# Performance work log

Hardware: AMD Instinct MI355X
Metric: run time of the kernel (lower is better)

## Reference

```python
import jax, jax.numpy as jnp
import numpy as np

# dims
H = 1024          # hidden_size
E = 2048          # d_inner = 2*H
NH = 32           # nheads = E/64
P = 64            # headdim
N = 128           # d_state
G = 1             # ngroups
K = 4             # d_conv
Q = 128           # SSD chunk length
FF = 4096         # intermediate_size
EPS = 1e-6        # rms_norm_eps
NEPS = 1e-5       # mamba gated-norm eps
CONV_DIM = E + 2 * G * N            # 2304
D_IN = 2 * E + 2 * G * N + NH       # 4384


def rmsnorm(x, w, eps):
    v = jnp.mean(x.astype(jnp.float32) ** 2, axis=-1, keepdims=True)
    return (x.astype(jnp.float32) * jax.lax.rsqrt(v + eps)).astype(x.dtype) * w


def segsum(x):
    # x: [..., T] -> [..., T, T] with out[i,j] = sum_{j<k<=i} x[k], -inf above diag
    T = x.shape[-1]
    cs = jnp.cumsum(x, axis=-1)
    s = cs[..., :, None] - cs[..., None, :]
    mask = jnp.tril(jnp.ones((T, T), dtype=bool))
    return jnp.where(mask, s, -jnp.inf)


def ssd(x, dt, A_log, B, C):
    # x:[b,l,nh,p], dt:[b,l,nh], B,C:[b,l,N] (ngroups=1, shared over heads)
    b, l, nh, p = x.shape
    A = -jnp.exp(A_log)                      # [nh]
    dA = dt * A                              # [b,l,nh]
    xd = x * dt[..., None]                   # discretized input
    c = l // Q
    xd = xd.reshape(b, c, Q, nh, p)
    dAc = dA.reshape(b, c, Q, nh).transpose(0, 3, 1, 2)   # [b,h,c,q]
    Bc = B.reshape(b, c, Q, N)
    Cc = C.reshape(b, c, Q, N)
    A_cs = jnp.cumsum(dAc, axis=-1)                        # [b,h,c,q]
    Lm = jnp.exp(segsum(dAc))                              # [b,h,c,q,q]
    # intra-chunk (diagonal blocks)
    Y_diag = jnp.einsum('bcqn,bcsn,bhcqs,bcshp->bcqhp', Cc, Bc, Lm, xd)
    # per-chunk final states
    decay_states = jnp.exp(A_cs[..., -1:] - A_cs)          # [b,h,c,q]
    states = jnp.einsum('bcqn,bhcq,bcqhp->bchpn', Bc, decay_states, xd)
    # inter-chunk recurrence (initial state = 0)
    A_last = jnp.pad(A_cs[..., -1], ((0, 0), (0, 0), (1, 0)))   # [b,h,c+1]
    decay_chunk = jnp.exp(segsum(A_last))                       # [b,h,c+1,c+1]
    states = jnp.concatenate([jnp.zeros_like(states[:, :1]), states], axis=1)
    new_states = jnp.einsum('bhzc,bchpn->bzhpn', decay_chunk, states)[:, :-1]
    Y_off = jnp.einsum('bcqn,bchpn,bhcq->bcqhp', Cc, new_states, jnp.exp(A_cs))
    return (Y_diag + Y_off).reshape(b, l, nh, p)


def mamba2(h, w_in, w_conv, b_conv, dt_bias, A_log, D, w_mnorm, w_out):
    b, l, _ = h.shape
    zxbcdt = h @ w_in.T                         # [b,l,D_IN]
    z, xBC, dt = jnp.split(zxbcdt, [E, E + CONV_DIM], axis=-1)
    # causal depthwise conv (kernel K) over channels of xBC
    pad = jnp.pad(xBC, ((0, 0), (K - 1, 0), (0, 0)))
    xBC = sum(pad[:, k:k + l, :] * w_conv[:, k] for k in range(K)) + b_conv
    xBC = jax.nn.silu(xBC)
    x, B, C = jnp.split(xBC, [E, E + G * N], axis=-1)
    dt = jax.nn.softplus(dt + dt_bias)          # [b,l,NH]
    xh = x.reshape(b, l, NH, P)
    y = ssd(xh, dt, A_log, B, C)
    y = y + D[None, None, :, None] * xh         # per-head skip
    y = y.reshape(b, l, E)
    y = rmsnorm(y * jax.nn.silu(z), w_mnorm, NEPS)   # gated RMSNorm
    return y @ w_out.T


def setup_inputs() -> dict:
    key = jax.random.key(0)
    ks = jax.random.split(key, 12)
    dt0 = jax.random.uniform(ks[0], (NH,), minval=0.001, maxval=0.1)
    dt_bias = dt0 + jnp.log(-jnp.expm1(-dt0))   # inverse softplus
    return {
        'hidden_states': jax.random.normal(ks[1], (2, 2048, H), dtype=jnp.float32),
        'w_ln1': jnp.ones((H,), jnp.float32),
        'w_in': 0.02 * jax.random.normal(ks[2], (D_IN, H), dtype=jnp.float32),
        'w_conv': 0.1 * jax.random.normal(ks[3], (CONV_DIM, K), dtype=jnp.float32),
        'b_conv': jnp.zeros((CONV_DIM,), jnp.float32),
        'dt_bias': dt_bias,
        'A_log': jnp.log(jax.random.uniform(ks[4], (NH,), minval=1.0, maxval=16.0)),
        'D': jnp.ones((NH,), jnp.float32),
        'w_mnorm': jnp.ones((E,), jnp.float32),
        'w_out': 0.02 * jax.random.normal(ks[5], (H, E), dtype=jnp.float32),
        'w_ln2': jnp.ones((H,), jnp.float32),
        'w_gate': 0.02 * jax.random.normal(ks[6], (FF, H), dtype=jnp.float32),
        'w_up': 0.02 * jax.random.normal(ks[7], (FF, H), dtype=jnp.float32),
        'w_down': 0.02 * jax.random.normal(ks[8], (H, FF), dtype=jnp.float32),
    }


def reference(hidden_states, w_ln1, w_in, w_conv, b_conv, dt_bias, A_log, D,
              w_mnorm, w_out, w_ln2, w_gate, w_up, w_down):
    residual = hidden_states
    h = rmsnorm(hidden_states, w_ln1, EPS)
    h = mamba2(h, w_in, w_conv, b_conv, dt_bias, A_log, D, w_mnorm, w_out)
    hidden = residual + h
    residual = hidden
    h = rmsnorm(hidden, w_ln2, EPS)
    h = (jax.nn.silu(h @ w_gate.T) * (h @ w_up.T)) @ w_down.T
    return residual + h
```

## Files before the change

### kernel.cpp

```cpp
#include <hip/hip_runtime.h>

#define DEV static __device__ __forceinline__

typedef short bf16x8 __attribute__((ext_vector_type(8)));
typedef float floatx4 __attribute__((ext_vector_type(4)));
typedef unsigned short ushort4v __attribute__((ext_vector_type(4)));
typedef unsigned short ushort8v __attribute__((ext_vector_type(8)));

DEV unsigned short f32_bf16(float f) {
  unsigned int u = __builtin_bit_cast(unsigned int, f);
  u = u + 0x7fffu + ((u >> 16) & 1u);
  return (unsigned short)(u >> 16);
}
DEV float bf2f(unsigned short u) {
  unsigned int v = ((unsigned int)u) << 16;
  return __builtin_bit_cast(float, v);
}
DEV float sigmoidf_(float x) { return 1.0f / (1.0f + __expf(-x)); }
DEV float siluf_(float x) { return x * sigmoidf_(x); }

#define GLD_LDS16(g, l)                                                              \
  __builtin_amdgcn_global_load_lds((const __attribute__((address_space(1))) void*)(g), \
                                   (__attribute__((address_space(3))) void*)(l), 16, 0, 0)

template <int MODE, int BN>
__global__ __launch_bounds__(256) void gemm128(
    const unsigned short* __restrict__ A, const unsigned short* __restrict__ B,
    void* __restrict__ Cv, const unsigned short* __restrict__ other,
    int K, int lda, int ldb, int ldc, long long bsA, long long bsB, long long bsC) {
  constexpr int NBG = BN / 64;
  constexpr int NJ = BN / 32;
  constexpr int BUFSZ = 4096 + BN * 32;
  __shared__ unsigned short S[2 * BUFSZ];
  A += (long long)blockIdx.z * bsA;
  B += (long long)blockIdx.z * bsB;
  const long long coff = (long long)blockIdx.z * bsC;
  const int tid = threadIdx.x;
  const int w = tid >> 6, lane = tid & 63;

  const int nbx = gridDim.x, nby = gridDim.y;
  const int GM = 4;
  int bid = blockIdx.y * nbx + blockIdx.x;
  int gid = bid / (GM * nbx);
  int rem = bid - gid * (GM * nbx);
  int gsz = min(GM, nby - gid * GM);
  int mtile = gid * GM + rem % gsz;
  int ntile = rem / gsz;
  const int m0 = mtile << 7, n0 = ntile * BN;

  const int srow = lane >> 2;
  const int schunk = ((lane & 3) ^ (srow & 3)) * 8;
  const unsigned short* ag0 = A + (long long)(m0 + w * 32 + srow) * lda + schunk;
  const unsigned short* ag1 = ag0 + (long long)16 * lda;
  const unsigned short* bgp[NBG];
#pragma unroll
  for (int ii = 0; ii < NBG; ++ii)
    bgp[ii] = B + (long long)(n0 + w * (BN / 4) + srow + 16 * ii) * ldb + schunk;

  auto STAGE = [&](int buf, int k0) {
    unsigned short* as_ = S + buf * BUFSZ;
    unsigned short* bs_ = as_ + 4096;
    GLD_LDS16(ag0 + k0, as_ + w * 1024 + lane * 8);
    GLD_LDS16(ag1 + k0, as_ + w * 1024 + lane * 8 + 512);
#pragma unroll
    for (int ii = 0; ii < NBG; ++ii)
      GLD_LDS16(bgp[ii] + k0, bs_ + w * (NBG * 512) + ii * 512 + lane * 8);
  };

  const int wr = (w >> 1) << 6;
  const int wc = (w & 1) * (BN / 2);
  const int fr = lane & 15;
  const int slot = (((lane >> 4) ^ (fr & 3))) << 3;
  const int r0 = (lane >> 4) << 2;

  floatx4 acc[4][NJ];
#pragma unroll
  for (int i = 0; i < 4; ++i)
#pragma unroll
    for (int j = 0; j < NJ; ++j) acc[i][j] = (floatx4){0.f, 0.f, 0.f, 0.f};

  const int nsteps = K >> 5;
  STAGE(0, 0);
  if (nsteps > 1) STAGE(1, 32);

  for (int t = 0; t < nsteps; ++t) {
    if (t < nsteps - 1) {
      if constexpr (NBG == 2) {
        asm volatile("s_waitcnt vmcnt(4)" ::: "memory");
      } else {
        asm volatile("s_waitcnt vmcnt(6)" ::: "memory");
      }
    } else {
      asm volatile("s_waitcnt vmcnt(0)" ::: "memory");
    }
    __builtin_amdgcn_s_barrier();
    __builtin_amdgcn_sched_barrier(0);
    const unsigned short* Ab = S + (t & 1) * BUFSZ;
    const unsigned short* Bb = Ab + 4096;
    bf16x8 af[4], bf_[NJ];
#pragma unroll
    for (int i = 0; i < 4; ++i)
      af[i] = *(const bf16x8*)(Ab + (wr + i * 16 + fr) * 32 + slot);
#pragma unroll
    for (int j = 0; j < NJ; ++j)
      bf_[j] = *(const bf16x8*)(Bb + (wc + j * 16 + fr) * 32 + slot);
#pragma unroll
    for (int i = 0; i < 4; ++i)
#pragma unroll
      for (int j = 0; j < NJ; ++j)
        acc[i][j] = __builtin_amdgcn_mfma_f32_16x16x32_bf16(af[i], bf_[j], acc[i][j], 0, 0, 0);
    __builtin_amdgcn_sched_barrier(0);
    __builtin_amdgcn_s_barrier();
    if (t + 2 < nsteps) STAGE(t & 1, (t + 2) * 32);
  }

  if constexpr (MODE == 0) {
#pragma unroll
    for (int i = 0; i < 4; ++i) {
#pragma unroll
      for (int j = 0; j < NJ; ++j) {
        long long base = (long long)(m0 + wr + i * 16 + r0) * ldc + (n0 + wc + j * 16 + fr);
#pragma unroll
        for (int r = 0; r < 4; ++r) {
          ((float*)Cv)[coff + base + (long long)r * ldc] = acc[i][j][r];
        }
      }
    }
  } else {
    constexpr int PAD = BN + 4;
    float* scr = (float*)S;
    const int row_l = tid >> 3;
    const int col0 = (tid & 7) * 8;
    __syncthreads();
#pragma unroll
    for (int pass = 0; pass < 4; ++pass) {
      if ((w >> 1) == (pass >> 1)) {
#pragma unroll
        for (int ii = 0; ii < 2; ++ii) {
          int i = (pass & 1) * 2 + ii;
          int rl = i * 16 + r0 - (pass & 1) * 32;
#pragma unroll
          for (int j = 0; j < NJ; ++j) {
            int col = wc + j * 16 + fr;
#pragma unroll
            for (int r = 0; r < 4; ++r) scr[(rl + r) * PAD + col] = acc[i][j][r];
          }
        }
      }
      __syncthreads();
      long long grow = m0 + pass * 32 + row_l;
      long long gbase = coff + grow * ldc + n0;
      const float* srow_p = scr + row_l * PAD;
#pragma unroll
      for (int k = 0; k < BN / 64; ++k) {
        int col = col0 + k * 64;
        float v[8];
        *(float4*)&v[0] = *(const float4*)(srow_p + col);
        *(float4*)&v[4] = *(const float4*)(srow_p + col + 4);
        ushort8v o;
        if constexpr (MODE == 2) {
          ushort8v uo = *(const ushort8v*)(other + gbase + col);
#pragma unroll
          for (int e = 0; e < 8; ++e) o[e] = f32_bf16(siluf_(v[e]) * bf2f(uo[e]));
        } else {
#pragma unroll
          for (int e = 0; e < 8; ++e) o[e] = f32_bf16(v[e]);
        }
        *(ushort8v*)((unsigned short*)Cv + gbase + col) = o;
      }
      __syncthreads();
    }
  }
}

__global__ __launch_bounds__(256, 2) void gemm128_dual(
    const unsigned short* __restrict__ A, const unsigned short* __restrict__ Bg,
    const unsigned short* __restrict__ Bu, unsigned short* __restrict__ C,
    int K, int lda, int ldb, int ldc) {
  __shared__ unsigned short S[2 * 12288];
  const int tid = threadIdx.x;
  const int w = tid >> 6, lane = tid & 63;
  const int nbx = gridDim.x, nby = gridDim.y;
  const int GM = 4;
  int bid = blockIdx.y * nbx + blockIdx.x;
  int gid = bid / (GM * nbx);
  int rem = bid - gid * (GM * nbx);
  int gsz = min(GM, nby - gid * GM);
  int mtile = gid * GM + rem % gsz;
  int ntile = rem / gsz;
  const int m0 = mtile << 7, n0 = ntile << 7;

  const int srow = lane >> 2;
  const int schunk = ((lane & 3) ^ (srow & 3)) * 8;
  const unsigned short* ag0 = A + (long long)(m0 + w * 32 + srow) * lda + schunk;
  const unsigned short* ag1 = ag0 + (long long)16 * lda;
  const unsigned short* gg0 = Bg + (long long)(n0 + w * 32 + srow) * ldb + schunk;
  const unsigned short* gg1 = gg0 + (long long)16 * ldb;
  const unsigned short* ug0 = Bu + (long long)(n0 + w * 32 + srow) * ldb + schunk;
  const unsigned short* ug1 = ug0 + (long long)16 * ldb;

  auto STAGE = [&](int buf, int k0) {
    unsigned short* as_ = S + buf * 12288;
    unsigned short* gs_ = as_ + 4096;
    unsigned short* us_ = as_ + 8192;
    GLD_LDS16(ag0 + k0, as_ + w * 1024 + lane * 8);
    GLD_LDS16(ag1 + k0, as_ + w * 1024 + lane * 8 + 512);
    GLD_LDS16(gg0 + k0, gs_ + w * 1024 + lane * 8);
    GLD_LDS16(gg1 + k0, gs_ + w * 1024 + lane * 8 + 512);
    GLD_LDS16(ug0 + k0, us_ + w * 1024 + lane * 8);
    GLD_LDS16(ug1 + k0, us_ + w * 1024 + lane * 8 + 512);
  };

  const int wr = (w >> 1) << 6;
  const int wc = (w & 1) << 6;
  const int fr = lane & 15;
  const int slot = (((lane >> 4) ^ (fr & 3))) << 3;
  const int r0 = (lane >> 4) << 2;

  floatx4 accg[4][4], accu[4][4];
#pragma unroll
  for (int i = 0; i < 4; ++i)
#pragma unroll
    for (int j = 0; j < 4; ++j) {
      accg[i][j] = (floatx4){0.f, 0.f, 0.f, 0.f};
      accu[i][j] = (floatx4){0.f, 0.f, 0.f, 0.f};
    }

  const int nsteps = K >> 5;
  STAGE(0, 0);
  if (nsteps > 1) STAGE(1, 32);

  for (int t = 0; t < nsteps; ++t) {
    if (t < nsteps - 1) {
      asm volatile("s_waitcnt vmcnt(6)" ::: "memory");
    } else {
      asm volatile("s_waitcnt vmcnt(0)" ::: "memory");
    }
    __builtin_amdgcn_s_barrier();
    __builtin_amdgcn_sched_barrier(0);
    const unsigned short* Ab = S + (t & 1) * 12288;
    const unsigned short* Gb = Ab + 4096;
    const unsigned short* Ub = Ab + 8192;
    bf16x8 af[4], gf[4], uf[4];
#pragma unroll
    for (int i = 0; i < 4; ++i)
      af[i] = *(const bf16x8*)(Ab + (wr + i * 16 + fr) * 32 + slot);
#pragma unroll
    for (int j = 0; j < 4; ++j) {
      gf[j] = *(const bf16x8*)(Gb + (wc + j * 16 + fr) * 32 + slot);
      uf[j] = *(const bf16x8*)(Ub + (wc + j * 16 + fr) * 32 + slot);
    }
#pragma unroll
    for (int i = 0; i < 4; ++i)
#pragma unroll
      for (int j = 0; j < 4; ++j) {
        accg[i][j] = __builtin_amdgcn_mfma_f32_16x16x32_bf16(af[i], gf[j], accg[i][j], 0, 0, 0);
        accu[i][j] = __builtin_amdgcn_mfma_f32_16x16x32_bf16(af[i], uf[j], accu[i][j], 0, 0, 0);
      }
    __builtin_amdgcn_sched_barrier(0);
    __builtin_amdgcn_s_barrier();
    if (t + 2 < nsteps) STAGE(t & 1, (t + 2) * 32);
  }

#pragma unroll
  for (int i = 0; i < 4; ++i)
#pragma unroll
    for (int j = 0; j < 4; ++j)
#pragma unroll
      for (int r = 0; r < 4; ++r) accg[i][j][r] = siluf_(accg[i][j][r]) * accu[i][j][r];

  constexpr int PAD = 132;
  float* scr = (float*)S;
  const int row_l = tid >> 3;
  const int col0 = (tid & 7) * 8;
  __syncthreads();
#pragma unroll
  for (int pass = 0; pass < 4; ++pass) {
    if ((w >> 1) == (pass >> 1)) {
#pragma unroll
      for (int ii = 0; ii < 2; ++ii) {
        int i = (pass & 1) * 2 + ii;
        int rl = i * 16 + r0 - (pass & 1) * 32;
#pragma unroll
        for (int j = 0; j < 4; ++j) {
          int col = wc + j * 16 + fr;
#pragma unroll
          for (int r = 0; r < 4; ++r) scr[(rl + r) * PAD + col] = accg[i][j][r];
        }
      }
    }
    __syncthreads();
    long long grow = m0 + pass * 32 + row_l;
    long long gbase = grow * (long long)ldc + n0;
    const float* srow_p = scr + row_l * PAD;
#pragma unroll
    for (int k = 0; k < 2; ++k) {
      int col = col0 + k * 64;
      float v[8];
      *(float4*)&v[0] = *(const float4*)(srow_p + col);
      *(float4*)&v[4] = *(const float4*)(srow_p + col + 4);
      ushort8v o;
#pragma unroll
      for (int e = 0; e < 8; ++e) o[e] = f32_bf16(v[e]);
      *(ushort8v*)(C + gbase + col) = o;
    }
    __syncthreads();
  }
}

template <int WM>
__global__ __launch_bounds__(256) void gemm_small_nt(
    const unsigned short* __restrict__ A, const unsigned short* __restrict__ B,
    float* __restrict__ C, int M, int N, int K, int lda, int ldb, int ldc) {
  const int w = threadIdx.x >> 6;
  const int lane = threadIdx.x & 63;
  const int lm = lane & 15;
  const int ko = (lane >> 4) << 3;
  const int bn0 = blockIdx.x << 6;
  const int m_base = blockIdx.y * (WM * 64) + w * (WM * 16);

  const unsigned short* arow[WM];
#pragma unroll
  for (int i = 0; i < WM; ++i) arow[i] = A + (long long)(m_base + i * 16 + lm) * lda + ko;
  int nv = (N - bn0) >> 4;
  nv = nv > 4 ? 4 : nv;
  const unsigned short* brow[4];
#pragma unroll
  for (int j = 0; j < 4; ++j) {
    int nr = bn0 + j * 16 + lm;
    brow[j] = B + (long long)(j < nv ? nr : 0) * ldb + ko;
  }
  floatx4 acc[WM][4];
#pragma unroll
  for (int i = 0; i < WM; ++i)
#pragma unroll
    for (int j = 0; j < 4; ++j) acc[i][j] = (floatx4){0.f, 0.f, 0.f, 0.f};
  for (int k0 = 0; k0 < K; k0 += 32) {
    bf16x8 a[WM];
#pragma unroll
    for (int i = 0; i < WM; ++i) a[i] = *(const bf16x8*)(arow[i] + k0);
#pragma unroll
    for (int j = 0; j < 4; ++j) {
      if (j < nv) {
        bf16x8 b = *(const bf16x8*)(brow[j] + k0);
#pragma unroll
        for (int i = 0; i < WM; ++i)
          acc[i][j] = __builtin_amdgcn_mfma_f32_16x16x32_bf16(a[i], b, acc[i][j], 0, 0, 0);
      }
    }
  }
  const int r0 = (lane >> 4) << 2;
#pragma unroll
  for (int i = 0; i < WM; ++i)
#pragma unroll
    for (int j = 0; j < 4; ++j)
      if (j < nv) {
        int col = bn0 + j * 16 + lm;
        long long base = (long long)(m_base + i * 16 + r0) * ldc + col;
#pragma unroll
        for (int r = 0; r < 4; ++r) C[base + (long long)r * ldc] = acc[i][j][r];
      }
}

__global__ __launch_bounds__(256) void wconv_all_k(
    const float* __restrict__ w_in, const float* __restrict__ w_gate,
    const float* __restrict__ w_up, const float* __restrict__ w_down,
    const float* __restrict__ w_out, unsigned short* __restrict__ d_in_,
    unsigned short* __restrict__ d_gate, unsigned short* __restrict__ d_up,
    unsigned short* __restrict__ d_down, unsigned short* __restrict__ d_out_) {
  long long j = (long long)blockIdx.x * 256 + threadIdx.x;
  const float* src;
  unsigned short* dst;
  if (j < 1122304) {
    src = w_in; dst = d_in_;
  } else if ((j -= 1122304) < 1048576) {
    src = w_gate; dst = d_gate;
  } else if ((j -= 1048576) < 1048576) {
    src = w_up; dst = d_up;
  } else if ((j -= 1048576) < 1048576) {
    src = w_down; dst = d_down;
  } else if ((j -= 1048576) < 524288) {
    src = w_out; dst = d_out_;
  } else {
    return;
  }
  float4 v = ((const float4*)src)[j];
  ushort4v o = {f32_bf16(v.x), f32_bf16(v.y), f32_bf16(v.z), f32_bf16(v.w)};
  ((ushort4v*)dst)[j] = o;
}

__global__ __launch_bounds__(256) void zero_out_k(float* __restrict__ o, long long n) {
  long long i = (long long)blockIdx.x * 256 + threadIdx.x;
  if (i < n) o[i] = 0.f;
}

__global__ __launch_bounds__(256) void rmsnorm1024_bf16_k(const float* __restrict__ x,
                                                          const float* __restrict__ w,
                                                          unsigned short* __restrict__ out,
                                                          float eps) {
  long long row = blockIdx.x;
  int t = threadIdx.x;
  float4 v = ((const float4*)(x + row * 1024))[t];
  float ss = v.x * v.x + v.y * v.y + v.z * v.z + v.w * v.w;
  __shared__ float red[4];
#pragma unroll
  for (int o = 32; o > 0; o >>= 1) ss += __shfl_down(ss, o, 64);
  if ((t & 63) == 0) red[t >> 6] = ss;
  __syncthreads();
  float tot = red[0] + red[1] + red[2] + red[3];
  float sc = rsqrtf(tot * (1.0f / 1024.0f) + eps);
  float4 wv = ((const float4*)w)[t];
  ushort4v o = {f32_bf16(v.x * sc * wv.x), f32_bf16(v.y * sc * wv.y),
                f32_bf16(v.z * sc * wv.z), f32_bf16(v.w * sc * wv.w)};
  ((ushort4v*)(out + row * 1024))[t] = o;
}

__global__ __launch_bounds__(256) void add_rmsnorm_k(const float* __restrict__ hs,
                                                     const float* __restrict__ parts,
                                                     long long pstride, int np,
                                                     const float* __restrict__ w,
                                                     float* __restrict__ mh,
                                                     unsigned short* __restrict__ h2, float eps) {
  long long row = blockIdx.x;
  int t = threadIdx.x;
  float4 v = ((const float4*)(hs + row * 1024))[t];
  for (int p = 0; p < np; ++p) {
    float4 u = ((const float4*)(parts + p * pstride + row * 1024))[t];
    v.x += u.x;
    v.y += u.y;
    v.z += u.z;
    v.w += u.w;
  }
  ((float4*)(mh + row * 1024))[t] = v;
  float ss = v.x * v.x + v.y * v.y + v.z * v.z + v.w * v.w;
  __shared__ float red[4];
#pragma unroll
  for (int o = 32; o > 0; o >>= 1) ss += __shfl_down(ss, o, 64);
  if ((t & 63) == 0) red[t >> 6] = ss;
  __syncthreads();
  float tot = red[0] + red[1] + red[2] + red[3];
  float sc = rsqrtf(tot * (1.0f / 1024.0f) + eps);
  float4 wv = ((const float4*)w)[t];
  ushort4v o = {f32_bf16(v.x * sc * wv.x), f32_bf16(v.y * sc * wv.y),
                f32_bf16(v.z * sc * wv.z), f32_bf16(v.w * sc * wv.w)};
  ((ushort4v*)(h2 + row * 1024))[t] = o;
}

__global__ __launch_bounds__(256) void addn_f32_k(const float* __restrict__ a,
                                                  const float* __restrict__ parts,
                                                  long long pstride, int np,
                                                  float* __restrict__ o, long long n4) {
  long long i = (long long)blockIdx.x * 256 + threadIdx.x;
  if (i < n4) {
    float4 x = ((const float4*)a)[i];
    for (int p = 0; p < np; ++p) {
      float4 u = ((const float4*)(parts + p * pstride))[i];
      x.x += u.x;
      x.y += u.y;
      x.z += u.z;
      x.w += u.w;
    }
    ((float4*)o)[i] = x;
  }
}

__global__ __launch_bounds__(256) void gated_rmsnorm2048_k(const unsigned short* __restrict__ y,
                                                           const unsigned short* __restrict__ z,
                                                           const float* __restrict__ w,
                                                           unsigned short* __restrict__ out,
                                                           float eps) {
  long long row = blockIdx.x;
  int t = threadIdx.x;
  ushort8v yv = ((const ushort8v*)(y + row * 2048))[t];
  ushort8v zv = ((const ushort8v*)(z + row * 2048))[t];
  float g[8];
  float ss = 0.f;
#pragma unroll
  for (int j = 0; j < 8; ++j) {
    g[j] = bf2f(yv[j]) * siluf_(bf2f(zv[j]));
    ss += g[j] * g[j];
  }
  __shared__ float red[4];
#pragma unroll
  for (int o = 32; o > 0; o >>= 1) ss += __shfl_down(ss, o, 64);
  if ((t & 63) == 0) red[t >> 6] = ss;
  __syncthreads();
  float tot = red[0] + red[1] + red[2] + red[3];
  float sc = rsqrtf(tot * (1.0f / 2048.0f) + eps);
  float ww[8];
  *(float4*)&ww[0] = ((const float4*)w)[2 * t];
  *(float4*)&ww[4] = ((const float4*)w)[2 * t + 1];
  ushort8v o;
#pragma unroll
  for (int j = 0; j < 8; ++j) o[j] = f32_bf16(g[j] * sc * ww[j]);
  ((ushort8v*)(out + row * 2048))[t] = o;
}

__global__ __launch_bounds__(256) void conv_silu_k(const unsigned short* __restrict__ xraw,
                                                   const float* __restrict__ wconv,
                                                   const float* __restrict__ bconv,
                                                   unsigned short* __restrict__ xBC) {
  long long f = (long long)blockIdx.x * 256 + threadIdx.x;
  if (f >= 4096LL * 288) return;
  int m = (int)(f / 288);
  int cb = (int)(f - (long long)m * 288);
  int l = m & 2047;
  int ch0 = cb << 3;
  float acc[8];
  float4 bc0 = ((const float4*)bconv)[cb * 2];
  float4 bc1 = ((const float4*)bconv)[cb * 2 + 1];
  acc[0] = bc0.x; acc[1] = bc0.y; acc[2] = bc0.z; acc[3] = bc0.w;
  acc[4] = bc1.x; acc[5] = bc1.y; acc[6] = bc1.z; acc[7] = bc1.w;
  float4 wv[8];
#pragma unroll
  for (int j = 0; j < 8; ++j) wv[j] = ((const float4*)wconv)[ch0 + j];
#pragma unroll
  for (int k = 0; k < 4; ++k) {
    int lk = l + k - 3;
    if (lk >= 0) {
      ushort8v xv = *(const ushort8v*)(xraw + (long long)(m + k - 3) * 2304 + ch0);
      acc[0] += bf2f(xv[0]) * ((const float*)&wv[0])[k];
      acc[1] += bf2f(xv[1]) * ((const float*)&wv[1])[k];
      acc[2] += bf2f(xv[2]) * ((const float*)&wv[2])[k];
      acc[3] += bf2f(xv[3]) * ((const float*)&wv[3])[k];
      acc[4] += bf2f(xv[4]) * ((const float*)&wv[4])[k];
      acc[5] += bf2f(xv[5]) * ((const float*)&wv[5])[k];
      acc[6] += bf2f(xv[6]) * ((const float*)&wv[6])[k];
      acc[7] += bf2f(xv[7]) * ((const float*)&wv[7])[k];
    }
  }
  ushort8v o;
#pragma unroll
  for (int j = 0; j < 8; ++j) o[j] = f32_bf16(siluf_(acc[j]));
  *(ushort8v*)(xBC + (long long)m * 2304 + ch0) = o;
}

__global__ __launch_bounds__(128) void dA_cumsum_k(const float* __restrict__ dtraw,
                                                   const float* __restrict__ dt_bias,
                                                   const float* __restrict__ A_log,
                                                   float* __restrict__ dt_s,
                                                   float* __restrict__ dA_cs) {
  int bi = blockIdx.x;
  int c = bi & 15, h = (bi >> 4) & 31, b = bi >> 9;
  int q = threadIdx.x;
  long long idx = ((long long)(b * 2048 + c * 128 + q)) * 32 + h;
  float xv = dtraw[idx] + dt_bias[h];
  float sp = xv > 20.f ? xv : log1pf(expf(xv));
  dt_s[idx] = sp;
  float A = -expf(A_log[h]);
  float v = sp * A;
  __shared__ float sbuf[128];
  sbuf[q] = v;
  __syncthreads();
  for (int off = 1; off < 128; off <<= 1) {
    float tv = (q >= off) ? sbuf[q - off] : 0.f;
    __syncthreads();
    sbuf[q] += tv;
    __syncthreads();
  }
  dA_cs[(long long)bi * 128 + q] = sbuf[q];
}

__global__ __launch_bounds__(256) void ssd_diag_states_k(
    const unsigned short* __restrict__ xBC, const float* __restrict__ dt_s,
    const float* __restrict__ dA_cs, const unsigned short* __restrict__ G,
    unsigned short* __restrict__ y, unsigned short* __restrict__ states) {
  __shared__ unsigned short Mz[128 * 136];
  __shared__ unsigned short xdT[64 * 136];
  __shared__ float Acs[128];
  __shared__ float wdec[128];
  const int bx = blockIdx.x;
  const int h = bx & 31, c = (bx >> 5) & 15, b = bx >> 9;
  const int t = threadIdx.x;
  const int w = t >> 6, lane = t & 63, fr = lane & 15, hi = lane >> 4;
  const long long rowbase = (long long)b * 2048 + c * 128;
  const long long abase = ((long long)((b * 32 + h) * 16 + c)) << 7;

  if (t < 128) {
    float a = dA_cs[abase + t];
    Acs[t] = a;
    wdec[t] = __expf(dA_cs[abase + 127] - a);
  }
  {
    int s = t >> 1, p0 = (t & 1) * 32;
    float dtv = dt_s[(rowbase + s) * 32 + h];
    const ushort8v* xv = (const ushort8v*)(xBC + (rowbase + s) * 2304 + h * 64 + p0);
#pragma unroll
    for (int i = 0; i < 4; ++i) {
      ushort8v vv = xv[i];
#pragma unroll
      for (int j = 0; j < 8; ++j) xdT[(p0 + i * 8 + j) * 136 + s] = f32_bf16(bf2f(vv[j]) * dtv);
    }
  }
  __syncthreads();
  {
    int q = t >> 1, s0 = (t & 1) * 64;
    float aq = Acs[q];
    const ushort8v* gv =
        (const ushort8v*)(G + (((long long)(b * 16 + c)) * 128 + q) * 128 + s0);
#pragma unroll
    for (int i = 0; i < 8; ++i) {
      ushort8v gg = gv[i];
      ushort8v mo;
#pragma unroll
      for (int j = 0; j < 8; ++j) {
        int s = s0 + i * 8 + j;
        float m = (s <= q) ? bf2f(gg[j]) * __expf(aq - Acs[s]) : 0.f;
        mo[j] = f32_bf16(m);
      }
      *(ushort8v*)(Mz + q * 136 + s0 + i * 8) = mo;
    }
  }
  __syncthreads();
  const int q0 = w << 5;
  {
    floatx4 acc[2][4];
#pragma unroll
    for (int i = 0; i < 2; ++i)
#pragma unroll
      for (int j = 0; j < 4; ++j) acc[i][j] = (floatx4){0.f, 0.f, 0.f, 0.f};
#pragma unroll
    for (int k0 = 0; k0 < 128; k0 += 32) {
      int kk = k0 + hi * 8;
      bf16x8 a0 = *(const bf16x8*)(Mz + (q0 + fr) * 136 + kk);
      bf16x8 a1 = *(const bf16x8*)(Mz + (q0 + 16 + fr) * 136 + kk);
      bf16x8 bf_[4];
#pragma unroll
      for (int j = 0; j < 4; ++j) bf_[j] = *(const bf16x8*)(xdT + (j * 16 + fr) * 136 + kk);
#pragma unroll
      for (int j = 0; j < 4; ++j) {
        acc[0][j] = __builtin_amdgcn_mfma_f32_16x16x32_bf16(a0, bf_[j], acc[0][j], 0, 0, 0);
        acc[1][j] = __builtin_amdgcn_mfma_f32_16x16x32_bf16(a1, bf_[j], acc[1][j], 0, 0, 0);
      }
    }
    __syncthreads();
    float* scr = (float*)Mz;
#pragma unroll
    for (int i = 0; i < 2; ++i)
#pragma unroll
      for (int r = 0; r < 4; ++r) {
        int q = q0 + i * 16 + hi * 4 + r;
#pragma unroll
        for (int j = 0; j < 4; ++j) scr[q * 68 + j * 16 + fr] = acc[i][j][r];
      }
    __syncthreads();
    {
      int row = t >> 1, colh = (t & 1) * 32;
      unsigned short* yrow = y + (rowbase + row) * 2048 + h * 64 + colh;
      const float* sp = scr + row * 68 + colh;
#pragma unroll
      for (int k = 0; k < 4; ++k) {
        float4 v0 = *(const float4*)(sp + k * 8);
        float4 v1 = *(const float4*)(sp + k * 8 + 4);
        ushort8v o = {f32_bf16(v0.x), f32_bf16(v0.y), f32_bf16(v0.z), f32_bf16(v0.w),
                      f32_bf16(v1.x), f32_bf16(v1.y), f32_bf16(v1.z), f32_bf16(v1.w)};
        *(ushort8v*)(yrow + k * 8) = o;
      }
    }
  }
  __syncthreads();
  {
    int s = t >> 1, n0 = (t & 1) * 64;
    float wd = wdec[s];
    const ushort8v* bv = (const ushort8v*)(xBC + (rowbase + s) * 2304 + 2048 + n0);
#pragma unroll
    for (int i = 0; i < 8; ++i) {
      ushort8v bb = bv[i];
#pragma unroll
      for (int j = 0; j < 8; ++j) Mz[(n0 + i * 8 + j) * 136 + s] = f32_bf16(bf2f(bb[j]) * wd);
    }
  }
  __syncthreads();
  {
    floatx4 acc[2][4];
#pragma unroll
    for (int i = 0; i < 2; ++i)
#pragma unroll
      for (int j = 0; j < 4; ++j) acc[i][j] = (floatx4){0.f, 0.f, 0.f, 0.f};
#pragma unroll
    for (int k0 = 0; k0 < 128; k0 += 32) {
      int kk = k0 + hi * 8;
      bf16x8 a0 = *(const bf16x8*)(Mz + (q0 + fr) * 136 + kk);
      bf16x8 a1 = *(const bf16x8*)(Mz + (q0 + 16 + fr) * 136 + kk);
      bf16x8 bf_[4];
#pragma unroll
      for (int j = 0; j < 4; ++j) bf_[j] = *(const bf16x8*)(xdT + (j * 16 + fr) * 136 + kk);
#pragma unroll
      for (int j = 0; j < 4; ++j) {
        acc[0][j] = __builtin_amdgcn_mfma_f32_16x16x32_bf16(a0, bf_[j], acc[0][j], 0, 0, 0);
        acc[1][j] = __builtin_amdgcn_mfma_f32_16x16x32_bf16(a1, bf_[j], acc[1][j], 0, 0, 0);
      }
    }
    __syncthreads();
    float* scr = (float*)Mz;
#pragma unroll
    for (int i = 0; i < 2; ++i)
#pragma unroll
      for (int j = 0; j < 4; ++j) {
        int p = j * 16 + fr;
        int n = q0 + i * 16 + hi * 4;
#pragma unroll
        for (int r = 0; r < 4; ++r) scr[p * 132 + n + r] = acc[i][j][r];
      }
    __syncthreads();
    {
      unsigned short* st = states + (long long)bx * 8192;
      int p = t >> 2, nh = (t & 3) * 32;
      unsigned short* strow = st + p * 128 + nh;
      const float* sp = scr + p * 132 + nh;
#pragma unroll
      for (int k = 0; k < 4; ++k) {
        float4 v0 = *(const float4*)(sp + k * 8);
        float4 v1 = *(const float4*)(sp + k * 8 + 4);
        ushort8v o = {f32_bf16(v0.x), f32_bf16(v0.y), f32_bf16(v0.z), f32_bf16(v0.w),
                      f32_bf16(v1.x), f32_bf16(v1.y), f32_bf16(v1.z), f32_bf16(v1.w)};
        *(ushort8v*)(strow + k * 8) = o;
      }
    }
  }
}

__global__ __launch_bounds__(256) void ssd_scan_k(const float* __restrict__ dA_cs,
                                                  unsigned short* __restrict__ states) {
  int seg = blockIdx.x & 3;
  int h = (blockIdx.x >> 2) & 31;
  int b = blockIdx.x >> 7;
  int t = threadIdx.x;
  int e0 = seg * 2048 + t * 8;
  float carry[8];
#pragma unroll
  for (int i = 0; i < 8; ++i) carry[i] = 0.f;
  for (int c = 0; c < 16; ++c) {
    long long base = ((long long)((b * 16 + c) * 32 + h)) * 8192;
    float dec = __expf(dA_cs[(((long long)((b * 32 + h) * 16 + c)) << 7) + 127]);
    ushort8v v = *(const ushort8v*)(states + base + e0);
    ushort8v o;
#pragma unroll
    for (int i = 0; i < 8; ++i) {
      float local = bf2f(v[i]);
      o[i] = f32_bf16(carry[i]);
      carry[i] = dec * carry[i] + local;
    }
    *(ushort8v*)(states + base + e0) = o;
  }
}

__global__ __launch_bounds__(256) void ssd_off_k(const unsigned short* __restrict__ xBC,
                                                 const float* __restrict__ dA_cs,
                                                 const unsigned short* __restrict__ states,
                                                 const float* __restrict__ Dvec,
                                                 unsigned short* __restrict__ y) {
  __shared__ float eA[128];
  __shared__ float scr[128 * 68];
  const int bx = blockIdx.x;
  const int h = bx & 31, c = (bx >> 5) & 15, b = bx >> 9;
  const int t = threadIdx.x;
  const int w = t >> 6, lane = t & 63, fr = lane & 15, hi = lane >> 4;
  const long long rowbase = (long long)b * 2048 + c * 128;
  const long long abase = ((long long)((b * 32 + h) * 16 + c)) << 7;
  if (t < 128) eA[t] = __expf(dA_cs[abase + t]);
  __syncthreads();

  const unsigned short* st = states + (long long)bx * 8192;
  const int q0 = w << 5;
  floatx4 acc[2][4];
#pragma unroll
  for (int i = 0; i < 2; ++i)
#pragma unroll
    for (int j = 0; j < 4; ++j) acc[i][j] = (floatx4){0.f, 0.f, 0.f, 0.f};

#pragma unroll
  for (int k0 = 0; k0 < 128; k0 += 32) {
    int kk = k0 + hi * 8;
    bf16x8 a0 = *(const bf16x8*)(xBC + (rowbase + q0 + fr) * 2304 + 2176 + kk);
    bf16x8 a1 = *(const bf16x8*)(xBC + (rowbase + q0 + 16 + fr) * 2304 + 2176 + kk);
    bf16x8 bf_[4];
#pragma unroll
    for (int j = 0; j < 4; ++j) bf_[j] = *(const bf16x8*)(st + (j * 16 + fr) * 128 + kk);
#pragma unroll
    for (int j = 0; j < 4; ++j) {
      acc[0][j] = __builtin_amdgcn_mfma_f32_16x16x32_bf16(a0, bf_[j], acc[0][j], 0, 0, 0);
      acc[1][j] = __builtin_amdgcn_mfma_f32_16x16x32_bf16(a1, bf_[j], acc[1][j], 0, 0, 0);
    }
  }

#pragma unroll
  for (int i = 0; i < 2; ++i)
#pragma unroll
    for (int r = 0; r < 4; ++r) {
      int q = q0 + i * 16 + hi * 4 + r;
#pragma unroll
      for (int j = 0; j < 4; ++j) scr[q * 68 + j * 16 + fr] = acc[i][j][r];
    }
  __syncthreads();
  {
    float Dh = Dvec[h];
    int row = t >> 1, colh = (t & 1) * 32;
    float e = eA[row];
    const unsigned short* xrow = xBC + (rowbase + row) * 2304 + h * 64 + colh;
    unsigned short* yrow = y + (rowbase + row) * 2048 + h * 64 + colh;
    const float* sp = scr + row * 68 + colh;
#pragma unroll
    for (int k = 0; k < 4; ++k) {
      ushort8v yv = *(const ushort8v*)(yrow + k * 8);
      ushort8v xv = *(const ushort8v*)(xrow + k * 8);
      float4 a0 = *(const float4*)(sp + k * 8);
      float4 a1 = *(const float4*)(sp + k * 8 + 4);
      float av[8] = {a0.x, a0.y, a0.z, a0.w, a1.x, a1.y, a1.z, a1.w};
      ushort8v o;
#pragma unroll
      for (int e2 = 0; e2 < 8; ++e2)
        o[e2] = f32_bf16(bf2f(yv[e2]) + e * av[e2] + Dh * bf2f(xv[e2]));
      *(ushort8v*)(yrow + k * 8) = o;
    }
  }
}

extern "C" void kernel_launch(void* const* d_in, const int* in_sizes, int n_in, void* d_out,
                              int out_size, void* d_ws, size_t ws_size, hipStream_t stream) {
  const float* hs = (const float*)d_in[0];
  const float* w_ln1 = (const float*)d_in[1];
  const float* w_in = (const float*)d_in[2];
  const float* w_conv = (const float*)d_in[3];
  const float* b_conv = (const float*)d_in[4];
  const float* dt_bias = (const float*)d_in[5];
  const float* A_log = (const float*)d_in[6];
  const float* Dvec = (const float*)d_in[7];
  const float* w_mnorm = (const float*)d_in[8];
  const float* w_out = (const float*)d_in[9];
  const float* w_ln2 = (const float*)d_in[10];
  const float* w_gate = (const float*)d_in[11];
  const float* w_up = (const float*)d_in[12];
  const float* w_down = (const float*)d_in[13];
  float* out = (float*)d_out;
  const int M = 4096;

  char* ws = (char*)d_ws;
  const size_t R0 = 0;
  const size_t R1 = 33554432;
  const size_t R1b = R1 + 33554432;
  const size_t R2 = 71303168;
  const size_t R3 = 90177536;
  const size_t R4 = 107544576;
  const size_t W0 = 108068864;
  const size_t NEED = 133234688;

  if (ws_size < NEED) {
    hipLaunchKernelGGL(zero_out_k, dim3((out_size + 255) / 256), dim3(256), 0, stream, out,
                       (long long)out_size);
    return;
  }

  unsigned short* z = (unsigned short*)(ws + R0);
  unsigned short* act = (unsigned short*)(ws + R0);
  float* oproj_parts = (float*)(ws + R0);
  unsigned short* xraw = (unsigned short*)(ws + R1);
  unsigned short* states = (unsigned short*)(ws + R1);
  unsigned short* ybuf = (unsigned short*)(ws + R1 + 16777216);
  float* down_parts = (float*)(ws + R1);
  unsigned short* wbf_out = (unsigned short*)(ws + R1b);
  unsigned short* xBC = (unsigned short*)(ws + R2);
  unsigned short* ygn = (unsigned short*)(ws + R2);
  unsigned short* h2 = (unsigned short*)(ws + R2);
  unsigned short* hnorm = (unsigned short*)(ws + R3);
  unsigned short* wbf_in = (unsigned short*)(ws + R3 + 8388608);
  float* dt_s = (float*)(ws + R3);
  float* dA_cs = (float*)(ws + R3 + 524288);
  unsigned short* Gbuf = (unsigned short*)(ws + R3 + 1048576);
  float* mh = (float*)(ws + R3);
  float* dtraw = (float*)(ws + R4);
  unsigned short* wbf_gate = (unsigned short*)(ws + W0);
  unsigned short* wbf_up = (unsigned short*)(ws + W0 + 8388608);
  unsigned short* wbf_down = (unsigned short*)(ws + W0 + 16777216);

  hipLaunchKernelGGL(rmsnorm1024_bf16_k, dim3(M), dim3(256), 0, stream, hs, w_ln1, hnorm, 1e-6f);
  hipLaunchKernelGGL(wconv_all_k, dim3(18720), dim3(256), 0, stream, w_in, w_gate, w_up, w_down,
                     w_out, wbf_in, wbf_gate, wbf_up, wbf_down, wbf_out);
  hipLaunchKernelGGL((gemm128<1, 128>), dim3(16, 32, 1), dim3(256), 0, stream, hnorm, wbf_in,
                     (void*)z, (const unsigned short*)nullptr, 1024, 1024, 1024, 2048, 0LL, 0LL,
                     0LL);
  hipLaunchKernelGGL((gemm128<1, 128>), dim3(18, 32, 1), dim3(256), 0, stream, hnorm,
                     wbf_in + 2048 * 1024, (void*)xraw, (const unsigned short*)nullptr, 1024, 1024,
                     1024, 2304, 0LL, 0LL, 0LL);
  hipLaunchKernelGGL((gemm_small_nt<1>), dim3(1, 64, 1), dim3(256), 0, stream, hnorm,
                     wbf_in + 4352 * 1024, dtraw, M, 32, 1024, 1024, 1024, 32);
  hipLaunchKernelGGL(conv_silu_k, dim3(4608), dim3(256), 0, stream, xraw, w_conv, b_conv, xBC);
  hipLaunchKernelGGL(dA_cumsum_k, dim3(1024), dim3(128), 0, stream, dtraw, dt_bias, A_log, dt_s,
                     dA_cs);
  hipLaunchKernelGGL((gemm128<1, 128>), dim3(1, 1, 32), dim3(256), 0, stream, xBC + 2176,
                     xBC + 2048, (void*)Gbuf, (const unsigned short*)nullptr, 128, 2304, 2304, 128,
                     294912LL, 294912LL, 16384LL);
  hipLaunchKernelGGL(ssd_diag_states_k, dim3(1024), dim3(256), 0, stream, xBC, dt_s, dA_cs, Gbuf,
                     ybuf, states);
  hipLaunchKernelGGL(ssd_scan_k, dim3(256), dim3(256), 0, stream, dA_cs, states);
  hipLaunchKernelGGL(ssd_off_k, dim3(1024), dim3(256), 0, stream, xBC, dA_cs, states, Dvec, ybuf);
  hipLaunchKernelGGL(gated_rmsnorm2048_k, dim3(M), dim3(256), 0, stream, ybuf, z, w_mnorm, ygn,
                     1e-5f);
  hipLaunchKernelGGL((gemm128<0, 128>), dim3(8, 32, 2), dim3(256), 0, stream, ygn, wbf_out,
                     (void*)oproj_parts, (const unsigned short*)nullptr, 1024, 2048, 2048, 1024,
                     1024LL, 1024LL, 4194304LL);
  hipLaunchKernelGGL(add_rmsnorm_k, dim3(M), dim3(256), 0, stream, hs, oproj_parts, 4194304LL, 2,
                     w_ln2, mh, h2, 1e-6f);
  hipLaunchKernelGGL(gemm128_dual, dim3(32, 32, 1), dim3(256), 0, stream, h2, wbf_gate, wbf_up,
                     act, 1024, 1024, 1024, 4096);
  hipLaunchKernelGGL((gemm128<0, 128>), dim3(8, 32, 2), dim3(256), 0, stream, act, wbf_down,
                     (void*)down_parts, (const unsigned short*)nullptr, 2048, 4096, 4096, 1024,
                     2048LL, 2048LL, 4194304LL);
  hipLaunchKernelGGL(addn_f32_k, dim3(4096), dim3(256), 0, stream, mh, down_parts, 4194304LL, 2,
                     out, 1048576LL);
}
```

Before: 511.9 us.

## Merge z/xBC in-proj GEMMs and triple-buffer the dual gate/up GEMM

The two input-projection GEMMs (z and xBC) become a single launch with a new epilogue mode that sends column tiles below 2048 to z and the rest to xraw, each with its own leading dimension. This saves one launch and fills the GPU with one larger grid. The dual gate/up GEMM moves from double to triple LDS buffering: the next-next stage is issued right after the top barrier, which removes the trailing barrier in each k-step. The cost is more LDS per block (about 72KB), which could limit occupancy. The old MODE 2 fused SiLU epilogue in gemm128 is removed.

```diff
diff --git a/kernel.cpp b/kernel.cpp
--- a/kernel.cpp
+++ b/kernel.cpp
@@ -127,6 +127,23 @@
       }
     }
   } else {
+    unsigned short* dst;
+    int ldd, ncol;
+    if constexpr (MODE == 3) {
+      if (n0 < 2048) {
+        dst = (unsigned short*)Cv;
+        ldd = 2048;
+        ncol = n0;
+      } else {
+        dst = (unsigned short*)const_cast<unsigned short*>(other);
+        ldd = 2304;
+        ncol = n0 - 2048;
+      }
+    } else {
+      dst = (unsigned short*)Cv;
+      ldd = ldc;
+      ncol = n0;
+    }
     constexpr int PAD = BN + 4;
     float* scr = (float*)S;
     const int row_l = tid >> 3;
@@ -149,7 +166,7 @@
       }
       __syncthreads();
       long long grow = m0 + pass * 32 + row_l;
-      long long gbase = coff + grow * ldc + n0;
+      long long gbase = coff + grow * (long long)ldd + ncol;
       const float* srow_p = scr + row_l * PAD;
 #pragma unroll
       for (int k = 0; k < BN / 64; ++k) {
@@ -158,15 +175,9 @@
         *(float4*)&v[0] = *(const float4*)(srow_p + col);
         *(float4*)&v[4] = *(const float4*)(srow_p + col + 4);
         ushort8v o;
-        if constexpr (MODE == 2) {
-          ushort8v uo = *(const ushort8v*)(other + gbase + col);
-#pragma unroll
-          for (int e = 0; e < 8; ++e) o[e] = f32_bf16(siluf_(v[e]) * bf2f(uo[e]));
-        } else {
-#pragma unroll
-          for (int e = 0; e < 8; ++e) o[e] = f32_bf16(v[e]);
-        }
-        *(ushort8v*)((unsigned short*)Cv + gbase + col) = o;
+#pragma unroll
+        for (int e = 0; e < 8; ++e) o[e] = f32_bf16(v[e]);
+        *(ushort8v*)(dst + gbase + col) = o;
       }
       __syncthreads();
     }
@@ -177,7 +188,7 @@
     const unsigned short* __restrict__ A, const unsigned short* __restrict__ Bg,
     const unsigned short* __restrict__ Bu, unsigned short* __restrict__ C,
     int K, int lda, int ldb, int ldc) {
-  __shared__ unsigned short S[2 * 12288];
+  __shared__ unsigned short S[3 * 12288];
   const int tid = threadIdx.x;
   const int w = tid >> 6, lane = tid & 63;
   const int nbx = gridDim.x, nby = gridDim.y;
@@ -230,6 +241,7 @@
   STAGE(0, 0);
   if (nsteps > 1) STAGE(1, 32);
 
+  int cur = 0, nxt2 = 2;
   for (int t = 0; t < nsteps; ++t) {
     if (t < nsteps - 1) {
       asm volatile("s_waitcnt vmcnt(6)" ::: "memory");
@@ -238,7 +250,9 @@
     }
     __builtin_amdgcn_s_barrier();
     __builtin_amdgcn_sched_barrier(0);
-    const unsigned short* Ab = S + (t & 1) * 12288;
+    if (t + 2 < nsteps) STAGE(nxt2, (t + 2) * 32);
+    __builtin_amdgcn_sched_barrier(0);
+    const unsigned short* Ab = S + cur * 12288;
     const unsigned short* Gb = Ab + 4096;
     const unsigned short* Ub = Ab + 8192;
     bf16x8 af[4], gf[4], uf[4];
@@ -258,8 +272,8 @@
         accu[i][j] = __builtin_amdgcn_mfma_f32_16x16x32_bf16(af[i], uf[j], accu[i][j], 0, 0, 0);
       }
     __builtin_amdgcn_sched_barrier(0);
-    __builtin_amdgcn_s_barrier();
-    if (t + 2 < nsteps) STAGE(t & 1, (t + 2) * 32);
+    cur = (cur == 2) ? 0 : cur + 1;
+    nxt2 = (nxt2 == 2) ? 0 : nxt2 + 1;
   }
 
 #pragma unroll
@@ -876,12 +890,8 @@
   hipLaunchKernelGGL(rmsnorm1024_bf16_k, dim3(M), dim3(256), 0, stream, hs, w_ln1, hnorm, 1e-6f);
   hipLaunchKernelGGL(wconv_all_k, dim3(18720), dim3(256), 0, stream, w_in, w_gate, w_up, w_down,
                      w_out, wbf_in, wbf_gate, wbf_up, wbf_down, wbf_out);
-  hipLaunchKernelGGL((gemm128<1, 128>), dim3(16, 32, 1), dim3(256), 0, stream, hnorm, wbf_in,
-                     (void*)z, (const unsigned short*)nullptr, 1024, 1024, 1024, 2048, 0LL, 0LL,
-                     0LL);
-  hipLaunchKernelGGL((gemm128<1, 128>), dim3(18, 32, 1), dim3(256), 0, stream, hnorm,
-                     wbf_in + 2048 * 1024, (void*)xraw, (const unsigned short*)nullptr, 1024, 1024,
-                     1024, 2304, 0LL, 0LL, 0LL);
+  hipLaunchKernelGGL((gemm128<3, 128>), dim3(34, 32, 1), dim3(256), 0, stream, hnorm, wbf_in,
+                     (void*)z, (const unsigned short*)xraw, 1024, 1024, 1024, 2048, 0LL, 0LL, 0LL);
   hipLaunchKernelGGL((gemm_small_nt<1>), dim3(1, 64, 1), dim3(256), 0, stream, hnorm,
                      wbf_in + 4352 * 1024, dtraw, M, 32, 1024, 1024, 1024, 32);
   hipLaunchKernelGGL(conv_silu_k, dim3(4608), dim3(256), 0, stream, xraw, w_conv, b_conv, xBC);
```

After: 510.3 us. Within noise of the previous version (-0.3%).
